# Performance work log

Measured on AMD Instinct MI355X. Metric: run time of the kernel, lower is better.

Reference implementation:

```python
import jax, jax.numpy as jnp
import numpy as np

B, S, D, H, F, E = 2, 1024, 1024, 16, 2048, 8
HD = D // H


def _ln(x, g, b, eps=1e-5):
    m = x.mean(-1, keepdims=True)
    v = ((x - m) ** 2).mean(-1, keepdims=True)
    return (x - m) / jnp.sqrt(v + eps) * g + b


def setup_inputs() -> dict:
    key = jax.random.key(0)
    ks = jax.random.split(key, 12)
    rn = lambda k, shp, s=0.02: jax.random.normal(k, shp, jnp.float32) * s
    return {
        'src': jax.random.normal(ks[0], (B, S, D), jnp.float32),
        'q_w': rn(ks[1], (D, D)),
        'k_w': rn(ks[2], (D, D)),
        'v_w': rn(ks[3], (D, D)),
        'out_w': rn(ks[4], (D, D)),
        'gate_w': rn(ks[5], (D, D)),
        'gate_b': rn(ks[6], (D,)),
        'scale_w': rn(ks[7], (H, HD)),
        'n1_g': jnp.ones((D,), jnp.float32),
        'n1_b': jnp.zeros((D,), jnp.float32),
        'n2_g': jnp.ones((D,), jnp.float32),
        'n2_b': jnp.zeros((D,), jnp.float32),
        'moe_gate_w': rn(ks[8], (D, E)),
        'moe_gate_b': jnp.zeros((E,), jnp.float32),
        'w1': rn(ks[9], (E, D, F)),
        'b1': jnp.zeros((E, F), jnp.float32),
        'ln_g': jnp.ones((E, F), jnp.float32),
        'ln_b': jnp.zeros((E, F), jnp.float32),
        'w2': rn(ks[10], (E, F, D)),
        'b2': jnp.zeros((E, D), jnp.float32),
        'res_scale': jnp.ones((E,), jnp.float32),
    }


def reference(src, q_w, k_w, v_w, out_w, gate_w, gate_b, scale_w,
              n1_g, n1_b, n2_g, n2_b, moe_gate_w, moe_gate_b,
              w1, b1, ln_g, ln_b, w2, b2, res_scale):
    b, s, d = src.shape
    h = scale_w.shape[0]
    hd = d // h
    # --- MemoAttention (gated, dynamically scaled), eval mode ---
    q = (src @ q_w).reshape(b, s, h, hd).transpose(0, 2, 1, 3)  # [b,h,s,hd]
    k = (src @ k_w).reshape(b, s, h, hd).transpose(0, 2, 1, 3)
    v = (src @ v_w).reshape(b, s, h, hd).transpose(0, 2, 1, 3)
    scores = jnp.einsum('bhqd,bhkd->bhqk', q, k) / np.float32(np.sqrt(hd))
    scale = jax.nn.sigmoid(jnp.einsum('bhsd,hd->bhs', q, scale_w)) * 2.0
    scores = scores * scale[..., None]
    aw = jax.nn.softmax(scores, axis=-1)
    out = jnp.einsum('bhqk,bhkd->bhqd', aw, v).transpose(0, 2, 1, 3).reshape(b, s, d)
    gate = jax.nn.sigmoid(out @ gate_w + gate_b)
    attn = (out * gate) @ out_w
    # --- residual + norm1 ---
    x = _ln(src + attn, n1_g, n1_b)
    # --- MoE FFN (top-2 routing; torch loop overwrites -> last (max-index) expert
    xr = x.reshape(-1, d)                      # [N, d]
    n = xr.shape[0]
    logits = xr @ moe_gate_w + moe_gate_b       # [N, E]
    top_v, top_i = jax.lax.top_k(logits, 2)
    wts = jax.nn.softmax(top_v, axis=-1)        # [N, 2]
    chosen = jnp.max(top_i, axis=-1)            # last-written expert per token

    def expert(W1, B1, G, Bt, W2, B2, rsc):
        hh = xr @ W1 + B1                       # [N, F]
        hh = jax.nn.gelu(_ln(hh, G, Bt), approximate=False)
        return (hh @ W2 + B2) * rsc + xr        # [N, d]

    outs = jax.vmap(expert)(w1, b1, ln_g, ln_b, w2, b2, res_scale)  # [E,N,d]
    sel = jnp.take_along_axis(outs.transpose(1, 0, 2), chosen[:, None, None], axis=1)[:, 0]
    moe = sel * jnp.sum(wts, axis=-1, keepdims=True)
    # --- residual + norm2 ---
    return _ln(x + moe.reshape(b, s, d), n2_g, n2_b)
```

## Files before the change

kernel.cpp:

```cpp
#include <hip/hip_runtime.h>


typedef _Float16 f16;
typedef _Float16 f16x8 __attribute__((ext_vector_type(8)));
typedef _Float16 f16x4 __attribute__((ext_vector_type(4)));
typedef float f32x4 __attribute__((ext_vector_type(4)));

constexpr int CS  = 1024;
constexpr int CD  = 1024;
constexpr int CH  = 16;
constexpr int CHD = 64;
constexpr int CF  = 2048;
constexpr int CE  = 8;
constexpr int CN  = 2048;
constexpr int CBH = 32;
constexpr int KS  = 512;
constexpr int MAXT = 24;

constexpr float LO_SCALE = 2048.f;
constexpr float LO_INV   = 1.f / 2048.f;

#define MFMA16(a, b, c) __builtin_amdgcn_mfma_f32_16x16x32_f16((a), (b), (c), 0, 0, 0)

#define TO_GBL(p) ((const __attribute__((address_space(1))) void*)(p))
#define TO_LDS(p) ((__attribute__((address_space(3))) void*)(p))
#define GLD16(g, l) __builtin_amdgcn_global_load_lds(TO_GBL(g), TO_LDS(l), 16, 0, 0)

__device__ __forceinline__ void fsplit(float v, f16 &hi, f16 &lo) {
  hi = (f16)v;
  lo = (f16)((v - (float)hi) * LO_SCALE);
}


__global__ void k_split_cvt(const float* __restrict__ in, f16* __restrict__ oh,
                            f16* __restrict__ ol, int n) {
  int i = (blockIdx.x * blockDim.x + threadIdx.x) * 4;
  if (i >= n) return;
  float4 v = *(const float4*)(in + i);
  float a[4] = {v.x, v.y, v.z, v.w};
  f16x4 vh, vl;
#pragma unroll
  for (int j = 0; j < 4; ++j) {
    f16 hi = (f16)a[j];
    vh[j] = hi;
    vl[j] = (f16)((a[j] - (float)hi) * LO_SCALE);
  }
  *(f16x4*)(oh + i) = vh;
  *(f16x4*)(ol + i) = vl;
}

__global__ __launch_bounds__(256) void k_transpose_split(
    const float* __restrict__ in, f16* __restrict__ oh,
    f16* __restrict__ ol, int R, int C) {
  __shared__ float t[64][65];
  const int z = blockIdx.z;
  const float* src = in + (size_t)z * R * C;
  f16* dh = oh + (size_t)z * R * C;
  f16* dl = ol ? ol + (size_t)z * R * C : nullptr;
  const int c0 = blockIdx.x * 64, r0 = blockIdx.y * 64;
  const int tt = threadIdx.x;
  const int lane = tt & 63, wv = tt >> 6;
#pragma unroll
  for (int i = 0; i < 16; ++i)
    t[wv + i * 4][lane] = src[(size_t)(r0 + wv + i * 4) * C + c0 + lane];
  __syncthreads();
  const int oc = tt >> 4;
  const int og = tt & 15;
#pragma unroll
  for (int cc = 0; cc < 64; cc += 16) {
    f16x4 vh, vl;
#pragma unroll
    for (int j = 0; j < 4; ++j) {
      const float v = t[og * 4 + j][cc + oc];
      f16 hi = (f16)v;
      vh[j] = hi;
      vl[j] = (f16)((v - (float)hi) * LO_SCALE);
    }
    const size_t idx = (size_t)(c0 + cc + oc) * R + r0 + og * 4;
    *(f16x4*)(dh + idx) = vh;
    if (dl) *(f16x4*)(dl + idx) = vl;
  }
}


template <bool SPLIT>
__device__ __forceinline__ void gemm_tile128(
    const f16* a0, const f16* a1, const f16* al0, const f16* al1,
    const f16* b0, const f16* b1, const f16* bl0, const f16* bl1,
    int K, f16* lds, f32x4 (&accm)[4][4], f32x4 (&accc)[4][4]) {
  constexpr int BUF = SPLIT ? 16384 : 8192;
  constexpr int BO  = SPLIT ? 8192 : 4096;
  const int t = threadIdx.x;
  const int lane = t & 63, wave = t >> 6;
  const int wm = wave >> 1, wn = wave & 1;
  const int m16 = lane & 15, quad = lane >> 4;
  int aoff[4], boff[4];
#pragma unroll
  for (int s = 0; s < 4; ++s) {
    const int ra = wm * 64 + s * 16 + m16;
    aoff[s] = ra * 32 + ((quad ^ ((ra >> 1) & 3)) * 8);
    const int rb = wn * 64 + s * 16 + m16;
    boff[s] = BO + rb * 32 + ((quad ^ ((rb >> 1) & 3)) * 8);
  }
  auto stage = [&](f16* buf) {
    GLD16(a0, buf + t * 8);
    GLD16(a1, buf + 2048 + t * 8);
    GLD16(b0, buf + BO + t * 8);
    GLD16(b1, buf + BO + 2048 + t * 8);
    if constexpr (SPLIT) {
      GLD16(al0, buf + 4096 + t * 8);
      GLD16(al1, buf + 6144 + t * 8);
      GLD16(bl0, buf + 12288 + t * 8);
      GLD16(bl1, buf + 14336 + t * 8);
      al0 += 32; al1 += 32; bl0 += 32; bl1 += 32;
    }
    a0 += 32; a1 += 32; b0 += 32; b1 += 32;
  };
  stage(lds);
  int cur = 0;
  for (int k = 0; k < K; k += 32) {
    __syncthreads();
    f16* buf = lds + cur * BUF;
    if (k + 32 < K) stage(lds + (cur ^ 1) * BUF);
    f16x8 af[4], alf[4];
#pragma unroll
    for (int s = 0; s < 4; ++s) {
      af[s] = *(const f16x8*)(buf + aoff[s]);
      if constexpr (SPLIT) alf[s] = *(const f16x8*)(buf + 4096 + aoff[s]);
    }
#pragma unroll
    for (int sn = 0; sn < 4; ++sn) {
      const f16x8 bf = *(const f16x8*)(buf + boff[sn]);
#pragma unroll
      for (int sm = 0; sm < 4; ++sm)
        accm[sm][sn] = MFMA16(af[sm], bf, accm[sm][sn]);
      if constexpr (SPLIT) {
        const f16x8 blf = *(const f16x8*)(buf + 4096 + boff[sn]);
#pragma unroll
        for (int sm = 0; sm < 4; ++sm)
          accc[sm][sn] = MFMA16(af[sm], blf, accc[sm][sn]);
#pragma unroll
        for (int sm = 0; sm < 4; ++sm)
          accc[sm][sn] = MFMA16(alf[sm], bf, accc[sm][sn]);
      }
    }
    cur ^= 1;
  }
}


__global__ __launch_bounds__(256, 2) void g_qkv(
    const f16* __restrict__ srcH, const f16* __restrict__ srcL,
    const f16* __restrict__ qwH, const f16* __restrict__ qwL,
    const f16* __restrict__ kwH, const f16* __restrict__ kwL,
    const f16* __restrict__ vwH, const f16* __restrict__ vwL,
    f16* __restrict__ qHo, f16* __restrict__ qLo,
    f16* __restrict__ kHo, f16* __restrict__ kLo,
    f16* __restrict__ vTH, f16* __restrict__ vTL) {
  __shared__ f16 lds[32768];
  const int z = blockIdx.z;
  const int m0 = blockIdx.x * 128, n0 = blockIdx.y * 128;
  const int t = threadIdx.x;
  const int rowS = t >> 2;
  const int ksw = ((t & 3) ^ ((rowS >> 1) & 3)) * 8;
  const f16* BH = (z == 0) ? qwH : (z == 1) ? kwH : vwH;
  const f16* BL = (z == 0) ? qwL : (z == 1) ? kwL : vwL;
  const f16* A0 = srcH + (size_t)(m0 + rowS) * CD + ksw;
  const f16* AL0 = srcL + (size_t)(m0 + rowS) * CD + ksw;
  const f16* B0 = BH + (size_t)(n0 + rowS) * CD + ksw;
  const f16* BL0 = BL + (size_t)(n0 + rowS) * CD + ksw;
  const f32x4 VZ = {0.f, 0.f, 0.f, 0.f};
  f32x4 accm[4][4], accc[4][4];
#pragma unroll
  for (int i = 0; i < 4; ++i)
#pragma unroll
    for (int j = 0; j < 4; ++j) { accm[i][j] = VZ; accc[i][j] = VZ; }
  gemm_tile128<true>(A0, A0 + (size_t)64 * CD, AL0, AL0 + (size_t)64 * CD,
                     B0, B0 + (size_t)64 * CD, BL0, BL0 + (size_t)64 * CD,
                     CD, lds, accm, accc);
  const int lane = t & 63, wave = t >> 6;
  const int wm = wave >> 1, wn = wave & 1;
  const int m16 = lane & 15, quad = lane >> 4;
  if (z == 2) {
#pragma unroll
    for (int sm = 0; sm < 4; ++sm)
#pragma unroll
      for (int sn = 0; sn < 4; ++sn) {
        const int row0 = m0 + wm * 64 + sm * 16 + quad * 4;
        const int col = n0 + wn * 64 + sn * 16 + m16;
        f16x4 vh, vl;
#pragma unroll
        for (int r = 0; r < 4; ++r) {
          const float v = accm[sm][sn][r] + accc[sm][sn][r] * LO_INV;
          f16 hi, lo; fsplit(v, hi, lo);
          vh[r] = hi; vl[r] = lo;
        }
        const int bb = row0 >> 10, ss = row0 & 1023;
        const int hh = col >> 6, hd = col & 63;
        const size_t idx = ((size_t)((bb * CH + hh) * CHD + hd)) * CS + ss;
        *(f16x4*)(vTH + idx) = vh;
        *(f16x4*)(vTL + idx) = vl;
      }
  } else {
#pragma unroll
    for (int sm = 0; sm < 4; ++sm)
#pragma unroll
      for (int sn = 0; sn < 4; ++sn)
#pragma unroll
        for (int r = 0; r < 4; ++r) {
          const int row = m0 + wm * 64 + sm * 16 + quad * 4 + r;
          const int col = n0 + wn * 64 + sn * 16 + m16;
          const float v = accm[sm][sn][r] + accc[sm][sn][r] * LO_INV;
          f16 hi, lo; fsplit(v, hi, lo);
          const int bb = row >> 10, ss = row & 1023;
          const int hh = col >> 6, hd = col & 63;
          const size_t idx = ((size_t)((bb * CH + hh) * CS + ss)) * CHD + hd;
          if (z == 0) { qHo[idx] = hi; qLo[idx] = lo; }
          else        { kHo[idx] = hi; kLo[idx] = lo; }
        }
  }
}


__device__ __forceinline__ int pswz(int q, int k) {
  return q * 64 + ((((k >> 2) ^ q) & 15) << 2) + (k & 3);
}

__global__ __launch_bounds__(256) void k_fattn(
    const f16* __restrict__ qH_, const f16* __restrict__ qL_,
    const f16* __restrict__ kH_, const f16* __restrict__ kL_,
    const f16* __restrict__ vTH_, const f16* __restrict__ vTL_,
    const float* __restrict__ scale_w,
    f16* __restrict__ aoH, f16* __restrict__ aoL) {
  __shared__ f16 kvb[32768];
  __shared__ float psc[4 * 1024];
  const int id = blockIdx.x + 16 * blockIdx.y;
  const int w = (id & 7) * 64 + (id >> 3);
  const int bh = w >> 4, qc = w & 15;
  const int b = bh >> 4, h = bh & 15;
  const int t = threadIdx.x;
  const int lane = t & 63, wave = t >> 6;
  const int m16 = lane & 15, quad = lane >> 4;
  const int q0 = qc * 64 + wave * 16;
  float* P = psc + wave * 1024;
  const f32x4 VZ = {0.f, 0.f, 0.f, 0.f};
  const size_t kb = (size_t)bh * CS * CHD;

  const int rowS = t >> 3, chS = t & 7;
  auto stage = [&](f16* dst, int kc) {
#pragma unroll
    for (int i = 0; i < 2; ++i) {
      const int row = rowS + 32 * i;
      const int sc = (chS ^ (row & 7)) * 8;
      GLD16(kH_ + kb + (size_t)(kc + row) * CHD + sc, dst + i * 2048 + t * 8);
      GLD16(kL_ + kb + (size_t)(kc + row) * CHD + sc, dst + 4096 + i * 2048 + t * 8);
      GLD16(vTH_ + kb + (size_t)row * CS + kc + sc, dst + 8192 + i * 2048 + t * 8);
      GLD16(vTL_ + kb + (size_t)row * CS + kc + sc, dst + 12288 + i * 2048 + t * 8);
    }
  };
  auto ldf = [&](const f16* piece, int r, int q) -> f16x8 {
    return *(const f16x8*)(piece + r * 64 + ((q ^ (r & 7)) * 8));
  };

  const f16* qrh = qH_ + ((size_t)bh * CS + q0 + m16) * CHD + quad * 8;
  const f16* qrl = qL_ + ((size_t)bh * CS + q0 + m16) * CHD + quad * 8;
  f16x8 a0h = *(const f16x8*)(qrh);
  f16x8 a1h = *(const f16x8*)(qrh + 32);
  f16x8 a0l = *(const f16x8*)(qrl);
  f16x8 a1l = *(const f16x8*)(qrl + 32);

  stage(kvb, 0);

  float qsr[4];
  {
    const float* sw = scale_w + h * CHD + quad * 8;
    float4 s0 = *(const float4*)(sw);
    float4 s1 = *(const float4*)(sw + 4);
    float4 s2 = *(const float4*)(sw + 32);
    float4 s3 = *(const float4*)(sw + 36);
    float sv[16] = {s0.x, s0.y, s0.z, s0.w, s1.x, s1.y, s1.z, s1.w,
                    s2.x, s2.y, s2.z, s2.w, s3.x, s3.y, s3.z, s3.w};
    float dot = 0.f;
#pragma unroll
    for (int j = 0; j < 8; ++j) {
      dot += ((float)a0h[j] + (float)a0l[j] * LO_INV) * sv[j];
      dot += ((float)a1h[j] + (float)a1l[j] * LO_INV) * sv[8 + j];
    }
    dot += __shfl_xor(dot, 16);
    dot += __shfl_xor(dot, 32);
    const float qsv = 2.f / (1.f + __expf(-dot)) * (0.125f * 1.44269504f);
#pragma unroll
    for (int r = 0; r < 4; ++r) qsr[r] = __shfl(qsv, quad * 4 + r);
  }

  f32x4 accm[4], accc[4];
#pragma unroll
  for (int tt = 0; tt < 4; ++tt) { accm[tt] = VZ; accc[tt] = VZ; }
  float mrun[4], lrun[4];
#pragma unroll
  for (int r = 0; r < 4; ++r) { mrun[r] = -1e30f; lrun[r] = 0.f; }

  int cur = 0;
  for (int kc = 0; kc < CS; kc += 64) {
    __syncthreads();
    const f16* kv = kvb + cur * 16384;
    if (kc + 64 < CS) stage(kvb + (cur ^ 1) * 16384, kc + 64);

    f32x4 st[4];
#pragma unroll
    for (int tt = 0; tt < 4; ++tt) {
      const int r = tt * 16 + m16;
      f16x8 b0h = ldf(kv,        r, quad);
      f16x8 b1h = ldf(kv,        r, quad + 4);
      f16x8 b0l = ldf(kv + 4096, r, quad);
      f16x8 b1l = ldf(kv + 4096, r, quad + 4);
      f32x4 am = VZ, ac1 = VZ, ac2 = VZ;
      am = MFMA16(a0h, b0h, am); am = MFMA16(a1h, b1h, am);
      ac1 = MFMA16(a0h, b0l, ac1); ac2 = MFMA16(a0l, b0h, ac2);
      ac1 = MFMA16(a1h, b1l, ac1); ac2 = MFMA16(a1l, b1h, ac2);
#pragma unroll
      for (int r4 = 0; r4 < 4; ++r4)
        st[tt][r4] = (am[r4] + (ac1[r4] + ac2[r4]) * LO_INV) * qsr[r4];
    }
    float mx[4];
    bool grow = false;
#pragma unroll
    for (int r = 0; r < 4; ++r) {
      float m = fmaxf(fmaxf(st[0][r], st[1][r]), fmaxf(st[2][r], st[3][r]));
#pragma unroll
      for (int msk = 8; msk >= 1; msk >>= 1) m = fmaxf(m, __shfl_xor(m, msk));
      mx[r] = m;
      grow = grow || (m > mrun[r]);
    }
    if (__any(grow)) {
#pragma unroll
      for (int r = 0; r < 4; ++r) {
        const float mnew = fmaxf(mrun[r], mx[r]);
        const float alpha = exp2f(mrun[r] - mnew);
        mrun[r] = mnew;
        lrun[r] *= alpha;
#pragma unroll
        for (int tt = 0; tt < 4; ++tt) {
          accm[tt][r] *= alpha;
          accc[tt][r] *= alpha;
        }
      }
    }
    float rs[4] = {0.f, 0.f, 0.f, 0.f};
#pragma unroll
    for (int tt = 0; tt < 4; ++tt)
#pragma unroll
      for (int r = 0; r < 4; ++r) {
        const float e = exp2f(st[tt][r] - mrun[r]);
        rs[r] += e;
        P[pswz(quad * 4 + r, tt * 16 + m16)] = e;
      }
#pragma unroll
    for (int r = 0; r < 4; ++r) {
#pragma unroll
      for (int msk = 8; msk >= 1; msk >>= 1) rs[r] += __shfl_xor(rs[r], msk);
      lrun[r] += rs[r];
    }
    f16x8 pah[2], pal[2];
#pragma unroll
    for (int c = 0; c < 2; ++c) {
      const int k0 = c * 32 + quad * 8;
      float4 p0 = *(const float4*)(P + pswz(m16, k0));
      float4 p1 = *(const float4*)(P + pswz(m16, k0 + 4));
      float pv[8] = {p0.x, p0.y, p0.z, p0.w, p1.x, p1.y, p1.z, p1.w};
#pragma unroll
      for (int j = 0; j < 8; ++j) {
        f16 hi = (f16)pv[j];
        pah[c][j] = hi;
        pal[c][j] = (f16)((pv[j] - (float)hi) * LO_SCALE);
      }
    }
#pragma unroll
    for (int c = 0; c < 2; ++c) {
      f16x8 vbh[4];
#pragma unroll
      for (int tt = 0; tt < 4; ++tt) {
        const int r = tt * 16 + m16;
        vbh[tt] = ldf(kv + 8192, r, quad + 4 * c);
        f16x8 vbl = ldf(kv + 12288, r, quad + 4 * c);
        accm[tt] = MFMA16(pah[c], vbh[tt], accm[tt]);
        accc[tt] = MFMA16(pah[c], vbl, accc[tt]);
      }
#pragma unroll
      for (int tt = 0; tt < 4; ++tt)
        accc[tt] = MFMA16(pal[c], vbh[tt], accc[tt]);
    }
    cur ^= 1;
  }
#pragma unroll
  for (int tt = 0; tt < 4; ++tt)
#pragma unroll
    for (int r = 0; r < 4; ++r) {
      const int row = q0 + quad * 4 + r;
      const float v = (accm[tt][r] + accc[tt][r] * LO_INV) / lrun[r];
      f16 hi, lo; fsplit(v, hi, lo);
      const size_t idx = ((size_t)(b * CS + row)) * CD + h * CHD + tt * 16 + m16;
      aoH[idx] = hi; aoL[idx] = lo;
    }
}


__global__ __launch_bounds__(256, 2) void g_gate(
    const f16* __restrict__ aoH, const f16* __restrict__ aoL,
    const f16* __restrict__ gwH, const f16* __restrict__ gwL,
    float* __restrict__ gpre ) {
  __shared__ f16 lds[32768];
  const int m0 = blockIdx.x * 128, n0 = blockIdx.y * 128, s = blockIdx.z;
  const int t = threadIdx.x;
  const int rowS = t >> 2;
  const int ksw = ((t & 3) ^ ((rowS >> 1) & 3)) * 8;
  const int k0 = s * KS;
  const f16* A0 = aoH + (size_t)(m0 + rowS) * CD + k0 + ksw;
  const f16* AL0 = aoL + (size_t)(m0 + rowS) * CD + k0 + ksw;
  const f16* B0 = gwH + (size_t)(n0 + rowS) * CD + k0 + ksw;
  const f16* BL0 = gwL + (size_t)(n0 + rowS) * CD + k0 + ksw;
  const f32x4 VZ = {0.f, 0.f, 0.f, 0.f};
  f32x4 accm[4][4], accc[4][4];
#pragma unroll
  for (int i = 0; i < 4; ++i)
#pragma unroll
    for (int j = 0; j < 4; ++j) { accm[i][j] = VZ; accc[i][j] = VZ; }
  gemm_tile128<true>(A0, A0 + (size_t)64 * CD, AL0, AL0 + (size_t)64 * CD,
                     B0, B0 + (size_t)64 * CD, BL0, BL0 + (size_t)64 * CD,
                     KS, lds, accm, accc);
  float* gp = gpre + (size_t)s * CN * CD;
  const int lane = t & 63, wave = t >> 6;
  const int wm = wave >> 1, wn = wave & 1;
  const int m16 = lane & 15, quad = lane >> 4;
#pragma unroll
  for (int sm = 0; sm < 4; ++sm)
#pragma unroll
    for (int sn = 0; sn < 4; ++sn)
#pragma unroll
      for (int r = 0; r < 4; ++r) {
        const int row = m0 + wm * 64 + sm * 16 + quad * 4 + r;
        const int col = n0 + wn * 64 + sn * 16 + m16;
        gp[(size_t)row * CD + col] = accm[sm][sn][r] + accc[sm][sn][r] * LO_INV;
      }
}

__global__ __launch_bounds__(256) void k_gatemul(
    const float* __restrict__ gpre, const f16* __restrict__ aoH,
    const f16* __restrict__ aoL, const float* __restrict__ gate_b,
    f16* __restrict__ gdH, f16* __restrict__ gdL) {
  const int i = (blockIdx.x * 256 + threadIdx.x) * 4;
  float4 p0 = *(const float4*)(gpre + i);
  float4 p1 = *(const float4*)(gpre + (size_t)CN * CD + i);
  float4 gb = *(const float4*)(gate_b + (i & (CD - 1)));
  f16x4 ah = *(const f16x4*)(aoH + i);
  f16x4 al = *(const f16x4*)(aoL + i);
  float pre[4] = {p0.x + p1.x + gb.x, p0.y + p1.y + gb.y,
                  p0.z + p1.z + gb.z, p0.w + p1.w + gb.w};
  f16x4 oh, ol;
#pragma unroll
  for (int j = 0; j < 4; ++j) {
    const float g = 1.f / (1.f + __expf(-pre[j]));
    const float ov = ((float)ah[j] + (float)al[j] * LO_INV) * g;
    f16 hi, lo; fsplit(ov, hi, lo);
    oh[j] = hi; ol[j] = lo;
  }
  *(f16x4*)(gdH + i) = oh;
  *(f16x4*)(gdL + i) = ol;
}

__global__ __launch_bounds__(256, 2) void g_outp(
    const f16* __restrict__ gdH, const f16* __restrict__ gdL,
    const f16* __restrict__ owH, const f16* __restrict__ owL,
    float* __restrict__ y1p ) {
  __shared__ f16 lds[32768];
  const int m0 = blockIdx.x * 128, n0 = blockIdx.y * 128, s = blockIdx.z;
  const int t = threadIdx.x;
  const int rowS = t >> 2;
  const int ksw = ((t & 3) ^ ((rowS >> 1) & 3)) * 8;
  const int k0 = s * KS;
  const f16* A0 = gdH + (size_t)(m0 + rowS) * CD + k0 + ksw;
  const f16* AL0 = gdL + (size_t)(m0 + rowS) * CD + k0 + ksw;
  const f16* B0 = owH + (size_t)(n0 + rowS) * CD + k0 + ksw;
  const f16* BL0 = owL + (size_t)(n0 + rowS) * CD + k0 + ksw;
  const f32x4 VZ = {0.f, 0.f, 0.f, 0.f};
  f32x4 accm[4][4], accc[4][4];
#pragma unroll
  for (int i = 0; i < 4; ++i)
#pragma unroll
    for (int j = 0; j < 4; ++j) { accm[i][j] = VZ; accc[i][j] = VZ; }
  gemm_tile128<true>(A0, A0 + (size_t)64 * CD, AL0, AL0 + (size_t)64 * CD,
                     B0, B0 + (size_t)64 * CD, BL0, BL0 + (size_t)64 * CD,
                     KS, lds, accm, accc);
  float* yp = y1p + (size_t)s * CN * CD;
  const int lane = t & 63, wave = t >> 6;
  const int wm = wave >> 1, wn = wave & 1;
  const int m16 = lane & 15, quad = lane >> 4;
#pragma unroll
  for (int sm = 0; sm < 4; ++sm)
#pragma unroll
    for (int sn = 0; sn < 4; ++sn)
#pragma unroll
      for (int r = 0; r < 4; ++r) {
        const int row = m0 + wm * 64 + sm * 16 + quad * 4 + r;
        const int col = n0 + wn * 64 + sn * 16 + m16;
        yp[(size_t)row * CD + col] = accm[sm][sn][r] + accc[sm][sn][r] * LO_INV;
      }
}


__device__ __forceinline__ void block_reduce2(float &s, float &ss, float* red) {
#pragma unroll
  for (int msk = 32; msk >= 1; msk >>= 1) {
    s += __shfl_xor(s, msk);
    ss += __shfl_xor(ss, msk);
  }
  const int wave = threadIdx.x >> 6, lane = threadIdx.x & 63;
  if (lane == 0) { red[wave] = s; red[4 + wave] = ss; }
  __syncthreads();
  s = red[0] + red[1] + red[2] + red[3];
  ss = red[4] + red[5] + red[6] + red[7];
}

__global__ __launch_bounds__(256) void k_ln1(
    const float* __restrict__ y1p, const float* __restrict__ srcp,
    const float* __restrict__ g, const float* __restrict__ bb,
    float* __restrict__ x, f16* __restrict__ xH) {
  __shared__ float red[8];
  const int n = blockIdx.x;
  const int t = threadIdx.x;
  const size_t off = (size_t)n * CD + t * 4;
  float4 v0 = *(const float4*)(y1p + off);
  float4 v1 = *(const float4*)(y1p + (size_t)CN * CD + off);
  float4 v2 = *(const float4*)(srcp + off);
  float a[4] = {v0.x + v1.x + v2.x, v0.y + v1.y + v2.y,
                v0.z + v1.z + v2.z, v0.w + v1.w + v2.w};
  float s = a[0] + a[1] + a[2] + a[3];
  float ss = a[0]*a[0] + a[1]*a[1] + a[2]*a[2] + a[3]*a[3];
  block_reduce2(s, ss, red);
  const float mean = s * (1.f / CD);
  const float var = ss * (1.f / CD) - mean * mean;
  const float rstd = rsqrtf(var + 1e-5f);
#pragma unroll
  for (int j = 0; j < 4; ++j) {
    const int d = t * 4 + j;
    const float val = (a[j] - mean) * rstd * g[d] + bb[d];
    x[(size_t)n * CD + d] = val;
    xH[(size_t)n * CD + d] = (f16)val;
  }
}

__global__ __launch_bounds__(256) void k_ln2(
    const float* __restrict__ zbp, const float* __restrict__ x,
    const float* __restrict__ b2, const float* __restrict__ rsc,
    const int* __restrict__ chosen,
    const float* __restrict__ g, const float* __restrict__ bb,
    float* __restrict__ outp) {
  __shared__ float red[8];
  const int n = blockIdx.x;
  const int e = chosen[n];
  const float rs = rsc[e];
  const int t = threadIdx.x;
  const size_t off = (size_t)n * CD + t * 4;
  float4 p0 = *(const float4*)(zbp + off);
  float4 p1 = *(const float4*)(zbp + (size_t)CN * CD + off);
  float4 p2 = *(const float4*)(zbp + (size_t)2 * CN * CD + off);
  float4 p3 = *(const float4*)(zbp + (size_t)3 * CN * CD + off);
  float4 xv = *(const float4*)(x + off);
  float4 bv = *(const float4*)(b2 + (size_t)e * CD + t * 4);
  float a[4] = {2.f * xv.x + (p0.x + p1.x + p2.x + p3.x + bv.x) * rs,
                2.f * xv.y + (p0.y + p1.y + p2.y + p3.y + bv.y) * rs,
                2.f * xv.z + (p0.z + p1.z + p2.z + p3.z + bv.z) * rs,
                2.f * xv.w + (p0.w + p1.w + p2.w + p3.w + bv.w) * rs};
  float s = a[0] + a[1] + a[2] + a[3];
  float ss = a[0]*a[0] + a[1]*a[1] + a[2]*a[2] + a[3]*a[3];
  block_reduce2(s, ss, red);
  const float mean = s * (1.f / CD);
  const float var = ss * (1.f / CD) - mean * mean;
  const float rstd = rsqrtf(var + 1e-5f);
#pragma unroll
  for (int j = 0; j < 4; ++j) {
    const int d = t * 4 + j;
    outp[(size_t)n * CD + d] = (a[j] - mean) * rstd * g[d] + bb[d];
  }
}


__global__ void k_zero_counts(int* counts) {
  if (threadIdx.x < CE) counts[threadIdx.x] = 0;
}

__global__ __launch_bounds__(256) void k_route(
    const float* __restrict__ x, const float* __restrict__ gw, const float* __restrict__ gb,
    int* __restrict__ chosen, int* __restrict__ counts, int* __restrict__ bucket) {
  const int wave = threadIdx.x >> 6, lane = threadIdx.x & 63;
  const int n = blockIdx.x * 4 + wave;
  const float* xr = x + (size_t)n * CD;
  float acc[CE];
#pragma unroll
  for (int e = 0; e < CE; ++e) acc[e] = 0.f;
  for (int j = 0; j < 16; ++j) {
    const int d = lane * 16 + j;
    const float xv = xr[d];
    const float* wr = gw + (size_t)d * CE;
#pragma unroll
    for (int e = 0; e < CE; ++e) acc[e] += xv * wr[e];
  }
#pragma unroll
  for (int msk = 32; msk >= 1; msk >>= 1) {
#pragma unroll
    for (int e = 0; e < CE; ++e) acc[e] += __shfl_xor(acc[e], msk);
  }
  if (lane == 0) {
    float best = -1e30f, second = -1e30f;
    int bi = 0, si = 0;
#pragma unroll
    for (int e = 0; e < CE; ++e) {
      const float L = acc[e] + gb[e];
      if (L > best) { second = best; si = bi; best = L; bi = e; }
      else if (L > second) { second = L; si = e; }
    }
    const int ch = bi > si ? bi : si;
    chosen[n] = ch;
    const int pos = atomicAdd(&counts[ch], 1);
    bucket[ch * CN + pos] = n;
  }
}

__global__ void k_plan(const int* __restrict__ counts, int* __restrict__ tiles) {
  if (threadIdx.x == 0) {
    int n = 0;
    for (int e = 0; e < CE; ++e) {
      const int c = counts[e];
      for (int m0 = 0; m0 < c; m0 += 128) { tiles[2 * n] = e; tiles[2 * n + 1] = m0; ++n; }
    }
    for (; n < MAXT; ++n) { tiles[2 * n] = -1; tiles[2 * n + 1] = 0; }
  }
}


__global__ __launch_bounds__(256, 2) void g_moe1(
    const f16* __restrict__ xH, const f16* __restrict__ w1t,
    const int* __restrict__ counts, const int* __restrict__ bucket,
    const int* __restrict__ tiles, float* __restrict__ hbp ) {
  const int e = tiles[2 * blockIdx.x];
  if (e < 0) return;
  const int m0 = tiles[2 * blockIdx.x + 1];
  const int cnt = counts[e];
  const int s = blockIdx.z;
  __shared__ f16 lds[16384];
  const int t = threadIdx.x;
  const int rowS = t >> 2;
  const int ksw = ((t & 3) ^ ((rowS >> 1) & 3)) * 8;
  const int k0 = s * KS;
  int ra0 = m0 + rowS;      if (ra0 > cnt - 1) ra0 = cnt - 1;
  int ra1 = m0 + rowS + 64; if (ra1 > cnt - 1) ra1 = cnt - 1;
  const int tok0 = bucket[e * CN + ra0];
  const int tok1 = bucket[e * CN + ra1];
  const int n0 = blockIdx.y * 128;
  const f16* B0 = w1t + ((size_t)e * CF + n0 + rowS) * CD + k0 + ksw;
  const f32x4 VZ = {0.f, 0.f, 0.f, 0.f};
  f32x4 accm[4][4], accd[4][4];
#pragma unroll
  for (int i = 0; i < 4; ++i)
#pragma unroll
    for (int j = 0; j < 4; ++j) { accm[i][j] = VZ; accd[i][j] = VZ; }
  gemm_tile128<false>(xH + (size_t)tok0 * CD + k0 + ksw,
                      xH + (size_t)tok1 * CD + k0 + ksw, nullptr, nullptr,
                      B0, B0 + (size_t)64 * CD, nullptr, nullptr,
                      KS, lds, accm, accd);
  float* hp = hbp + (size_t)s * CN * CF;
  const int lane = t & 63, wave = t >> 6;
  const int wm = wave >> 1, wn = wave & 1;
  const int m16 = lane & 15, quad = lane >> 4;
#pragma unroll
  for (int sm = 0; sm < 4; ++sm)
#pragma unroll
    for (int sn = 0; sn < 4; ++sn)
#pragma unroll
      for (int r = 0; r < 4; ++r) {
        const int rr = m0 + wm * 64 + sm * 16 + quad * 4 + r;
        if (rr >= cnt) continue;
        const int tok = bucket[e * CN + rr];
        const int col = n0 + wn * 64 + sn * 16 + m16;
        hp[(size_t)tok * CF + col] = accm[sm][sn][r];
      }
}

__global__ __launch_bounds__(256) void k_lngelu(
    const float* __restrict__ hbp, const int* __restrict__ chosen,
    const float* __restrict__ b1,
    const float* __restrict__ ln_g, const float* __restrict__ ln_b,
    f16* __restrict__ h2) {
  __shared__ float red[8];
  const int n = blockIdx.x;
  const int e = chosen[n];
  const int t = threadIdx.x;
  const size_t off = (size_t)n * CF + t * 8;
  float4 v0 = *(const float4*)(hbp + off);
  float4 v1 = *(const float4*)(hbp + off + 4);
  float4 u0 = *(const float4*)(hbp + (size_t)CN * CF + off);
  float4 u1 = *(const float4*)(hbp + (size_t)CN * CF + off + 4);
  float4 b0 = *(const float4*)(b1 + (size_t)e * CF + t * 8);
  float4 b1v = *(const float4*)(b1 + (size_t)e * CF + t * 8 + 4);
  float a[8] = {v0.x + u0.x + b0.x, v0.y + u0.y + b0.y,
                v0.z + u0.z + b0.z, v0.w + u0.w + b0.w,
                v1.x + u1.x + b1v.x, v1.y + u1.y + b1v.y,
                v1.z + u1.z + b1v.z, v1.w + u1.w + b1v.w};
  float s = 0.f, ss = 0.f;
#pragma unroll
  for (int j = 0; j < 8; ++j) { s += a[j]; ss += a[j] * a[j]; }
  block_reduce2(s, ss, red);
  const float mean = s * (1.f / CF);
  const float var = ss * (1.f / CF) - mean * mean;
  const float rstd = rsqrtf(var + 1e-5f);
  const float* g = ln_g + (size_t)e * CF;
  const float* bb = ln_b + (size_t)e * CF;
#pragma unroll
  for (int j = 0; j < 8; ++j) {
    const int d = t * 8 + j;
    const float val = (a[j] - mean) * rstd * g[d] + bb[d];
    const float gl = 0.5f * val * (1.f + erff(val * 0.70710678118654752f));
    h2[(size_t)n * CF + d] = (f16)gl;
  }
}

__global__ __launch_bounds__(256, 2) void g_moe2(
    const f16* __restrict__ h2, const f16* __restrict__ w2t,
    const int* __restrict__ counts, const int* __restrict__ bucket,
    const int* __restrict__ tiles, float* __restrict__ zbp ) {
  const int e = tiles[2 * blockIdx.x];
  if (e < 0) return;
  const int m0 = tiles[2 * blockIdx.x + 1];
  const int cnt = counts[e];
  const int s = blockIdx.z;
  __shared__ f16 lds[16384];
  const int t = threadIdx.x;
  const int rowS = t >> 2;
  const int ksw = ((t & 3) ^ ((rowS >> 1) & 3)) * 8;
  const int k0 = s * KS;
  int ra0 = m0 + rowS;      if (ra0 > cnt - 1) ra0 = cnt - 1;
  int ra1 = m0 + rowS + 64; if (ra1 > cnt - 1) ra1 = cnt - 1;
  const int tok0 = bucket[e * CN + ra0];
  const int tok1 = bucket[e * CN + ra1];
  const int n0 = blockIdx.y * 128;
  const f16* B0 = w2t + ((size_t)e * CD + n0 + rowS) * CF + k0 + ksw;
  const f32x4 VZ = {0.f, 0.f, 0.f, 0.f};
  f32x4 accm[4][4], accd[4][4];
#pragma unroll
  for (int i = 0; i < 4; ++i)
#pragma unroll
    for (int j = 0; j < 4; ++j) { accm[i][j] = VZ; accd[i][j] = VZ; }
  gemm_tile128<false>(h2 + (size_t)tok0 * CF + k0 + ksw,
                      h2 + (size_t)tok1 * CF + k0 + ksw, nullptr, nullptr,
                      B0, B0 + (size_t)64 * CF, nullptr, nullptr,
                      KS, lds, accm, accd);
  float* zp = zbp + (size_t)s * CN * CD;
  const int lane = t & 63, wave = t >> 6;
  const int wm = wave >> 1, wn = wave & 1;
  const int m16 = lane & 15, quad = lane >> 4;
#pragma unroll
  for (int sm = 0; sm < 4; ++sm)
#pragma unroll
    for (int sn = 0; sn < 4; ++sn)
#pragma unroll
      for (int r = 0; r < 4; ++r) {
        const int rr = m0 + wm * 64 + sm * 16 + quad * 4 + r;
        if (rr >= cnt) continue;
        const int tok = bucket[e * CN + rr];
        const int col = n0 + wn * 64 + sn * 16 + m16;
        zp[(size_t)tok * CD + col] = accm[sm][sn][r];
      }
}


extern "C" void kernel_launch(void* const* d_in, const int* in_sizes, int n_in,
                              void* d_out, int out_size, void* d_ws, size_t ws_size,
                              hipStream_t stream) {
  (void)in_sizes; (void)n_in; (void)out_size; (void)ws_size;
  const float* src        = (const float*)d_in[0];
  const float* q_w        = (const float*)d_in[1];
  const float* k_w        = (const float*)d_in[2];
  const float* v_w        = (const float*)d_in[3];
  const float* out_w      = (const float*)d_in[4];
  const float* gate_w     = (const float*)d_in[5];
  const float* gate_b     = (const float*)d_in[6];
  const float* scale_w    = (const float*)d_in[7];
  const float* n1_g       = (const float*)d_in[8];
  const float* n1_b       = (const float*)d_in[9];
  const float* n2_g       = (const float*)d_in[10];
  const float* n2_b       = (const float*)d_in[11];
  const float* moe_gate_w = (const float*)d_in[12];
  const float* moe_gate_b = (const float*)d_in[13];
  const float* w1         = (const float*)d_in[14];
  const float* b1         = (const float*)d_in[15];
  const float* ln_g       = (const float*)d_in[16];
  const float* ln_b       = (const float*)d_in[17];
  const float* w2         = (const float*)d_in[18];
  const float* b2         = (const float*)d_in[19];
  const float* res_scale  = (const float*)d_in[20];
  float* outp = (float*)d_out;

  char* p = (char*)d_ws;
  auto take = [&](size_t bytes) -> char* {
    char* r = p;
    p += (bytes + 255) & ~(size_t)255;
    return r;
  };
  f16* srcH = (f16*)take((size_t)CN * CD * 2);
  f16* srcL = (f16*)take((size_t)CN * CD * 2);
  f16* qwH = (f16*)take((size_t)CD * CD * 2);
  f16* qwL = (f16*)take((size_t)CD * CD * 2);
  f16* kwH = (f16*)take((size_t)CD * CD * 2);
  f16* kwL = (f16*)take((size_t)CD * CD * 2);
  f16* vwH = (f16*)take((size_t)CD * CD * 2);
  f16* vwL = (f16*)take((size_t)CD * CD * 2);
  f16* gwH = (f16*)take((size_t)CD * CD * 2);
  f16* gwL = (f16*)take((size_t)CD * CD * 2);
  f16* owH = (f16*)take((size_t)CD * CD * 2);
  f16* owL = (f16*)take((size_t)CD * CD * 2);
  f16* qH = (f16*)take((size_t)CBH * CS * CHD * 2);
  f16* qL = (f16*)take((size_t)CBH * CS * CHD * 2);
  f16* kH = (f16*)take((size_t)CBH * CS * CHD * 2);
  f16* kL = (f16*)take((size_t)CBH * CS * CHD * 2);
  f16* vTH = (f16*)take((size_t)CBH * CS * CHD * 2);
  f16* vTL = (f16*)take((size_t)CBH * CS * CHD * 2);
  f16* aoH = (f16*)take((size_t)CN * CD * 2);
  f16* aoL = (f16*)take((size_t)CN * CD * 2);
  f16* gdH = (f16*)take((size_t)CN * CD * 2);
  f16* gdL = (f16*)take((size_t)CN * CD * 2);
  float* x  = (float*)take((size_t)CN * CD * 4);
  f16* xH = (f16*)take((size_t)CN * CD * 2);
  int* counts = (int*)take(64);
  int* bucket = (int*)take((size_t)CE * CN * 4);
  int* chosen = (int*)take((size_t)CN * 4);
  int* tiles = (int*)take((size_t)MAXT * 2 * 4);
  f16* h2 = (f16*)take((size_t)CN * CF * 2);
  f16* w1t = (f16*)take((size_t)CE * CF * CD * 2);
  f16* w2t = (f16*)take((size_t)CE * CD * CF * 2);
  float* pbuf = (float*)take((size_t)4 * CN * CD * 4);

  k_split_cvt<<<dim3(CN * CD / 4 / 256), 256, 0, stream>>>(src, srcH, srcL, CN * CD);
  k_transpose_split<<<dim3(CD / 64, CD / 64, 1), 256, 0, stream>>>(q_w, qwH, qwL, CD, CD);
  k_transpose_split<<<dim3(CD / 64, CD / 64, 1), 256, 0, stream>>>(k_w, kwH, kwL, CD, CD);
  k_transpose_split<<<dim3(CD / 64, CD / 64, 1), 256, 0, stream>>>(v_w, vwH, vwL, CD, CD);
  k_transpose_split<<<dim3(CD / 64, CD / 64, 1), 256, 0, stream>>>(gate_w, gwH, gwL, CD, CD);
  k_transpose_split<<<dim3(CD / 64, CD / 64, 1), 256, 0, stream>>>(out_w, owH, owL, CD, CD);
  k_transpose_split<<<dim3(CF / 64, CD / 64, CE), 256, 0, stream>>>(w1, w1t, nullptr, CD, CF);
  k_transpose_split<<<dim3(CD / 64, CF / 64, CE), 256, 0, stream>>>(w2, w2t, nullptr, CF, CD);

  g_qkv<<<dim3(CN / 128, CD / 128, 3), 256, 0, stream>>>(
      srcH, srcL, qwH, qwL, kwH, kwL, vwH, vwL, qH, qL, kH, kL, vTH, vTL);
  k_fattn<<<dim3(CS / 64, CBH), 256, 0, stream>>>(
      qH, qL, kH, kL, vTH, vTL, scale_w, aoH, aoL);
  g_gate<<<dim3(CN / 128, CD / 128, 2), 256, 0, stream>>>(aoH, aoL, gwH, gwL, pbuf);
  k_gatemul<<<dim3(CN * CD / 4 / 256), 256, 0, stream>>>(pbuf, aoH, aoL, gate_b, gdH, gdL);
  g_outp<<<dim3(CN / 128, CD / 128, 2), 256, 0, stream>>>(gdH, gdL, owH, owL, pbuf);
  k_ln1<<<dim3(CN), 256, 0, stream>>>(pbuf, src, n1_g, n1_b, x, xH);

  k_zero_counts<<<dim3(1), 64, 0, stream>>>(counts);
  k_route<<<dim3(CN / 4), 256, 0, stream>>>(x, moe_gate_w, moe_gate_b, chosen, counts, bucket);
  k_plan<<<dim3(1), 64, 0, stream>>>(counts, tiles);
  g_moe1<<<dim3(MAXT, CF / 128, 2), 256, 0, stream>>>(xH, w1t, counts, bucket, tiles, pbuf);
  k_lngelu<<<dim3(CN), 256, 0, stream>>>(pbuf, chosen, b1, ln_g, ln_b, h2);
  g_moe2<<<dim3(MAXT, CD / 128, 4), 256, 0, stream>>>(h2, w2t, counts, bucket, tiles, pbuf);
  k_ln2<<<dim3(CN), 256, 0, stream>>>(pbuf, x, b2, res_scale, chosen, n2_g, n2_b, outp);
}
```

Measured before the change: 522.3 us.

## Drop split-fp16 low part for V and P in attention; batch weight transposes

```diff
diff --git a/kernel.cpp b/kernel.cpp
--- a/kernel.cpp
+++ b/kernel.cpp
@@ -82,6 +82,45 @@
   }
 }
 
+__global__ __launch_bounds__(256) void k_transpose5(
+    const float* __restrict__ s0, const float* __restrict__ s1,
+    const float* __restrict__ s2, const float* __restrict__ s3,
+    const float* __restrict__ s4,
+    f16* __restrict__ h0, f16* __restrict__ l0,
+    f16* __restrict__ h1, f16* __restrict__ l1,
+    f16* __restrict__ h2, f16* __restrict__ l2,
+    f16* __restrict__ h3, f16* __restrict__ l3,
+    f16* __restrict__ h4, f16* __restrict__ l4) {
+  __shared__ float t[64][65];
+  const int z = blockIdx.z;
+  const float* src = (z == 0) ? s0 : (z == 1) ? s1 : (z == 2) ? s2 : (z == 3) ? s3 : s4;
+  f16* dh = (z == 0) ? h0 : (z == 1) ? h1 : (z == 2) ? h2 : (z == 3) ? h3 : h4;
+  f16* dl = (z == 0) ? l0 : (z == 1) ? l1 : (z == 2) ? l2 : (z == 3) ? l3 : l4;
+  const int c0 = blockIdx.x * 64, r0 = blockIdx.y * 64;
+  const int tt = threadIdx.x;
+  const int lane = tt & 63, wv = tt >> 6;
+#pragma unroll
+  for (int i = 0; i < 16; ++i)
+    t[wv + i * 4][lane] = src[(size_t)(r0 + wv + i * 4) * CD + c0 + lane];
+  __syncthreads();
+  const int oc = tt >> 4;
+  const int og = tt & 15;
+#pragma unroll
+  for (int cc = 0; cc < 64; cc += 16) {
+    f16x4 vh, vl;
+#pragma unroll
+    for (int j = 0; j < 4; ++j) {
+      const float v = t[og * 4 + j][cc + oc];
+      f16 hi = (f16)v;
+      vh[j] = hi;
+      vl[j] = (f16)((v - (float)hi) * LO_SCALE);
+    }
+    const size_t idx = (size_t)(c0 + cc + oc) * CD + r0 + og * 4;
+    *(f16x4*)(dh + idx) = vh;
+    *(f16x4*)(dl + idx) = vl;
+  }
+}
+
 
 template <bool SPLIT>
 __device__ __forceinline__ void gemm_tile128(
@@ -156,7 +195,7 @@
     const f16* __restrict__ vwH, const f16* __restrict__ vwL,
     f16* __restrict__ qHo, f16* __restrict__ qLo,
     f16* __restrict__ kHo, f16* __restrict__ kLo,
-    f16* __restrict__ vTH, f16* __restrict__ vTL) {
+    f16* __restrict__ vTH) {
   __shared__ f16 lds[32768];
   const int z = blockIdx.z;
   const int m0 = blockIdx.x * 128, n0 = blockIdx.y * 128;
@@ -188,18 +227,14 @@
       for (int sn = 0; sn < 4; ++sn) {
         const int row0 = m0 + wm * 64 + sm * 16 + quad * 4;
         const int col = n0 + wn * 64 + sn * 16 + m16;
-        f16x4 vh, vl;
-#pragma unroll
-        for (int r = 0; r < 4; ++r) {
-          const float v = accm[sm][sn][r] + accc[sm][sn][r] * LO_INV;
-          f16 hi, lo; fsplit(v, hi, lo);
-          vh[r] = hi; vl[r] = lo;
-        }
+        f16x4 vh;
+#pragma unroll
+        for (int r = 0; r < 4; ++r)
+          vh[r] = (f16)(accm[sm][sn][r] + accc[sm][sn][r] * LO_INV);
         const int bb = row0 >> 10, ss = row0 & 1023;
         const int hh = col >> 6, hd = col & 63;
         const size_t idx = ((size_t)((bb * CH + hh) * CHD + hd)) * CS + ss;
         *(f16x4*)(vTH + idx) = vh;
-        *(f16x4*)(vTL + idx) = vl;
       }
   } else {
 #pragma unroll
@@ -229,10 +264,10 @@
 __global__ __launch_bounds__(256) void k_fattn(
     const f16* __restrict__ qH_, const f16* __restrict__ qL_,
     const f16* __restrict__ kH_, const f16* __restrict__ kL_,
-    const f16* __restrict__ vTH_, const f16* __restrict__ vTL_,
+    const f16* __restrict__ vTH_,
     const float* __restrict__ scale_w,
     f16* __restrict__ aoH, f16* __restrict__ aoL) {
-  __shared__ f16 kvb[32768];
+  __shared__ f16 kvb[24576];
   __shared__ float psc[4 * 1024];
   const int id = blockIdx.x + 16 * blockIdx.y;
   const int w = (id & 7) * 64 + (id >> 3);
@@ -255,7 +290,6 @@
       GLD16(kH_ + kb + (size_t)(kc + row) * CHD + sc, dst + i * 2048 + t * 8);
       GLD16(kL_ + kb + (size_t)(kc + row) * CHD + sc, dst + 4096 + i * 2048 + t * 8);
       GLD16(vTH_ + kb + (size_t)row * CS + kc + sc, dst + 8192 + i * 2048 + t * 8);
-      GLD16(vTL_ + kb + (size_t)row * CS + kc + sc, dst + 12288 + i * 2048 + t * 8);
     }
   };
   auto ldf = [&](const f16* piece, int r, int q) -> f16x8 {
@@ -293,9 +327,9 @@
     for (int r = 0; r < 4; ++r) qsr[r] = __shfl(qsv, quad * 4 + r);
   }
 
-  f32x4 accm[4], accc[4];
-#pragma unroll
-  for (int tt = 0; tt < 4; ++tt) { accm[tt] = VZ; accc[tt] = VZ; }
+  f32x4 accm[4];
+#pragma unroll
+  for (int tt = 0; tt < 4; ++tt) accm[tt] = VZ;
   float mrun[4], lrun[4];
 #pragma unroll
   for (int r = 0; r < 4; ++r) { mrun[r] = -1e30f; lrun[r] = 0.f; }
@@ -303,8 +337,8 @@
   int cur = 0;
   for (int kc = 0; kc < CS; kc += 64) {
     __syncthreads();
-    const f16* kv = kvb + cur * 16384;
-    if (kc + 64 < CS) stage(kvb + (cur ^ 1) * 16384, kc + 64);
+    const f16* kv = kvb + cur * 12288;
+    if (kc + 64 < CS) stage(kvb + (cur ^ 1) * 12288, kc + 64);
 
     f32x4 st[4];
 #pragma unroll
@@ -340,10 +374,7 @@
         mrun[r] = mnew;
         lrun[r] *= alpha;
 #pragma unroll
-        for (int tt = 0; tt < 4; ++tt) {
-          accm[tt][r] *= alpha;
-          accc[tt][r] *= alpha;
-        }
+        for (int tt = 0; tt < 4; ++tt) accm[tt][r] *= alpha;
       }
     }
     float rs[4] = {0.f, 0.f, 0.f, 0.f};
@@ -361,7 +392,7 @@
       for (int msk = 8; msk >= 1; msk >>= 1) rs[r] += __shfl_xor(rs[r], msk);
       lrun[r] += rs[r];
     }
-    f16x8 pah[2], pal[2];
+    f16x8 pah[2];
 #pragma unroll
     for (int c = 0; c < 2; ++c) {
       const int k0 = c * 32 + quad * 8;
@@ -369,27 +400,16 @@
       float4 p1 = *(const float4*)(P + pswz(m16, k0 + 4));
       float pv[8] = {p0.x, p0.y, p0.z, p0.w, p1.x, p1.y, p1.z, p1.w};
 #pragma unroll
-      for (int j = 0; j < 8; ++j) {
-        f16 hi = (f16)pv[j];
-        pah[c][j] = hi;
-        pal[c][j] = (f16)((pv[j] - (float)hi) * LO_SCALE);
-      }
-    }
-#pragma unroll
-    for (int c = 0; c < 2; ++c) {
-      f16x8 vbh[4];
+      for (int j = 0; j < 8; ++j) pah[c][j] = (f16)pv[j];
+    }
+#pragma unroll
+    for (int c = 0; c < 2; ++c)
 #pragma unroll
       for (int tt = 0; tt < 4; ++tt) {
         const int r = tt * 16 + m16;
-        vbh[tt] = ldf(kv + 8192, r, quad + 4 * c);
-        f16x8 vbl = ldf(kv + 12288, r, quad + 4 * c);
-        accm[tt] = MFMA16(pah[c], vbh[tt], accm[tt]);
-        accc[tt] = MFMA16(pah[c], vbl, accc[tt]);
+        f16x8 vbh = ldf(kv + 8192, r, quad + 4 * c);
+        accm[tt] = MFMA16(pah[c], vbh, accm[tt]);
       }
-#pragma unroll
-      for (int tt = 0; tt < 4; ++tt)
-        accc[tt] = MFMA16(pal[c], vbh[tt], accc[tt]);
-    }
     cur ^= 1;
   }
 #pragma unroll
@@ -397,7 +417,7 @@
 #pragma unroll
     for (int r = 0; r < 4; ++r) {
       const int row = q0 + quad * 4 + r;
-      const float v = (accm[tt][r] + accc[tt][r] * LO_INV) / lrun[r];
+      const float v = accm[tt][r] / lrun[r];
       f16 hi, lo; fsplit(v, hi, lo);
       const size_t idx = ((size_t)(b * CS + row)) * CD + h * CHD + tt * 16 + m16;
       aoH[idx] = hi; aoL[idx] = lo;
@@ -823,7 +843,6 @@
   f16* kH = (f16*)take((size_t)CBH * CS * CHD * 2);
   f16* kL = (f16*)take((size_t)CBH * CS * CHD * 2);
   f16* vTH = (f16*)take((size_t)CBH * CS * CHD * 2);
-  f16* vTL = (f16*)take((size_t)CBH * CS * CHD * 2);
   f16* aoH = (f16*)take((size_t)CN * CD * 2);
   f16* aoL = (f16*)take((size_t)CN * CD * 2);
   f16* gdH = (f16*)take((size_t)CN * CD * 2);
@@ -840,18 +859,16 @@
   float* pbuf = (float*)take((size_t)4 * CN * CD * 4);
 
   k_split_cvt<<<dim3(CN * CD / 4 / 256), 256, 0, stream>>>(src, srcH, srcL, CN * CD);
-  k_transpose_split<<<dim3(CD / 64, CD / 64, 1), 256, 0, stream>>>(q_w, qwH, qwL, CD, CD);
-  k_transpose_split<<<dim3(CD / 64, CD / 64, 1), 256, 0, stream>>>(k_w, kwH, kwL, CD, CD);
-  k_transpose_split<<<dim3(CD / 64, CD / 64, 1), 256, 0, stream>>>(v_w, vwH, vwL, CD, CD);
-  k_transpose_split<<<dim3(CD / 64, CD / 64, 1), 256, 0, stream>>>(gate_w, gwH, gwL, CD, CD);
-  k_transpose_split<<<dim3(CD / 64, CD / 64, 1), 256, 0, stream>>>(out_w, owH, owL, CD, CD);
+  k_transpose5<<<dim3(CD / 64, CD / 64, 5), 256, 0, stream>>>(
+      q_w, k_w, v_w, gate_w, out_w,
+      qwH, qwL, kwH, kwL, vwH, vwL, gwH, gwL, owH, owL);
   k_transpose_split<<<dim3(CF / 64, CD / 64, CE), 256, 0, stream>>>(w1, w1t, nullptr, CD, CF);
   k_transpose_split<<<dim3(CD / 64, CF / 64, CE), 256, 0, stream>>>(w2, w2t, nullptr, CF, CD);
 
   g_qkv<<<dim3(CN / 128, CD / 128, 3), 256, 0, stream>>>(
-      srcH, srcL, qwH, qwL, kwH, kwL, vwH, vwL, qH, qL, kH, kL, vTH, vTL);
+      srcH, srcL, qwH, qwL, kwH, kwL, vwH, vwL, qH, qL, kH, kL, vTH);
   k_fattn<<<dim3(CS / 64, CBH), 256, 0, stream>>>(
-      qH, qL, kH, kL, vTH, vTL, scale_w, aoH, aoL);
+      qH, qL, kH, kL, vTH, scale_w, aoH, aoL);
   g_gate<<<dim3(CN / 128, CD / 128, 2), 256, 0, stream>>>(aoH, aoL, gwH, gwL, pbuf);
   k_gatemul<<<dim3(CN * CD / 4 / 256), 256, 0, stream>>>(pbuf, aoH, aoL, gate_b, gdH, gdL);
   g_outp<<<dim3(CN / 128, CD / 128, 2), 256, 0, stream>>>(gdH, gdL, owH, owL, pbuf);
```

Result: faster. 497.8 us (-4.7%).
